# Optimization experiments

Hardware: AMD Instinct MI355X
Metric: run time of the kernel (lower is better)

## Reference

```python
import jax, jax.numpy as jnp
import numpy as np

EPS = 1e-6

def _ln(x, g, b):
    mu = jnp.mean(x, axis=-1, keepdims=True)
    var = jnp.mean(jnp.square(x - mu), axis=-1, keepdims=True)
    return (x - mu) * jax.lax.rsqrt(var + EPS) * g + b

def setup_inputs() -> dict:
    key = jax.random.key(0)
    ks = jax.random.split(key, 8)
    B, T, D = 4, 4096, 1024
    H = 16
    Dff = 4 * D
    s = 1.0 / np.sqrt(D)
    sf = 1.0 / np.sqrt(Dff)
    return {
        "x": jax.random.normal(ks[0], (B, T, D), dtype=jnp.float32),
        "wq": jax.random.uniform(ks[1], (D, D), jnp.float32, -s, s),
        "wk": jax.random.uniform(ks[2], (D, D), jnp.float32, -s, s),
        "wv": jax.random.uniform(ks[3], (D, D), jnp.float32, -s, s),
        "wo": jax.random.uniform(ks[4], (D, D), jnp.float32, -s, s),
        "ln1_g": jnp.ones((D,), jnp.float32),
        "ln1_b": jnp.zeros((D,), jnp.float32),
        "w1": jax.random.uniform(ks[5], (D, Dff), jnp.float32, -s, s),
        "b1": jnp.zeros((Dff,), jnp.float32),
        "w2": jax.random.uniform(ks[6], (Dff, D), jnp.float32, -sf, sf),
        "b2": jnp.zeros((D,), jnp.float32),
        "ln2_g": jnp.ones((D,), jnp.float32),
        "ln2_b": jnp.zeros((D,), jnp.float32),
    }

def reference(x, wq, wk, wv, wo, ln1_g, ln1_b, w1, b1, w2, b2, ln2_g, ln2_b):
    B, T, D = x.shape
    H = 16
    dk = D // H
    x1 = _ln(x, ln1_g, ln1_b)
    q = (x1 @ wq).reshape(B, T, H, dk)
    k = (x1 @ wk).reshape(B, T, H, dk)
    v = (x1 @ wv).reshape(B, T, H, dk)
    # NOTE: faithful to source -- attention mixes HEADS at each token position
    # attn[b,t,h,g] = softmax_g( sum_d q[b,t,h,d]*k[b,t,g,d] / sqrt(dk) )
    attn = jax.nn.softmax(jnp.einsum('bthd,btgd->bthg', q / np.sqrt(dk), k), axis=-1)
    o = jnp.einsum('bthg,btgd->bthd', attn, v)
    # faithful head-major reshape: transpose(1,2).contiguous().view(B,T,-1)
    o = jnp.transpose(o, (0, 2, 1, 3)).reshape(B, T, H * dk)
    o = o @ wo
    q2 = _ln(o + x, ln1_g, ln1_b)  # same layer_norm params reused
    h = jax.nn.gelu(q2 @ w1 + b1, approximate=False)
    y = h @ w2 + b2 + q2
    return _ln(y, ln2_g, ln2_b)
```

## Files before the change

kernel.cpp:

```cpp
#include <hip/hip_runtime.h>


typedef __attribute__((ext_vector_type(8))) short s16x8;
typedef __attribute__((ext_vector_type(4))) short s16x4;
typedef __attribute__((ext_vector_type(4))) float f32x4;

__device__ __forceinline__ short f2bf(float x) {
  unsigned u = __builtin_bit_cast(unsigned, x);
  u = (u + 0x7FFFu + ((u >> 16) & 1u)) >> 16;
  return (short)u;
}
__device__ __forceinline__ float bf2f(short s) {
  unsigned u = ((unsigned)(unsigned short)s) << 16;
  return __builtin_bit_cast(float, u);
}

__device__ __forceinline__ void ld_g2l16(const short* g, const short* l) {
  __builtin_amdgcn_global_load_lds(
      (const __attribute__((address_space(1))) void*)g,
      (__attribute__((address_space(3))) void*)l, 16, 0, 0);
}

__device__ __forceinline__ s16x8 lds_read8(const short* smem, int off) {
  const __attribute__((address_space(3))) short* p =
      (const __attribute__((address_space(3))) short*)smem;
  return *(const __attribute__((address_space(3))) s16x8*)(p + off);
}

__device__ __forceinline__ float fast_gelu(float v) {
  float y = 0.7978845608f * (v + 0.044715f * v * v * v);
  float ay = fabsf(y);
  float t = __expf(-2.0f * ay);
  float th = (1.0f - t) * __frcp_rn(1.0f + t);
  th = (y >= 0.f) ? th : -th;
  return 0.5f * v * (1.0f + th);
}

#define MFMA16(va, vb, vc) \
  __builtin_amdgcn_mfma_f32_16x16x32_bf16(va, vb, vc, 0, 0, 0)

template <int EPI>
__global__ __launch_bounds__(512, 2) void gemm256(
    const short* __restrict__ A, const short* __restrict__ BT,
    void* __restrict__ outp, const float* __restrict__ bias, int N, int K) {
  extern __shared__ __align__(16) short smem[];

  const int t = threadIdx.x;
  const int lane = t & 63, w = t >> 6;
  const int wm = w >> 2, wn = w & 3;

  const int nbn = N >> 8;
  const int oi = (int)blockIdx.x;
  const int seq = oi >> 3;
  const int bq = seq / nbn;
  const int bm = (oi & 7) * 8 + bq;
  const int bn = seq - bq * nbn;

  const int l8 = lane >> 3;
  const int lcw = ((lane & 7) ^ l8) * 8;
  const short* gA = A + (size_t)(bm * 256 + w * 8 + l8) * K + lcw;
  const short* gB = BT + (size_t)(bn * 256 + w * 8 + l8) * K + lcw;
  const int lb = w * 512;

  auto stage = [&](const short* g, int bufo, int h, int kt) {
    const int go = h * 128 * K + kt * 64;
    ld_g2l16(g + go, smem + bufo + h * 8192 + lb);
    ld_g2l16(g + go + 64 * K, smem + bufo + h * 8192 + 4096 + lb);
  };

  const int fr = lane & 15, fc = lane >> 4;
  const int baseA = (wm * 128 + fr) * 64;
  const int baseB = (wn * 64 + fr) * 64;
  const int sl0 = (fc ^ (fr & 7)) * 8;
  const int sl1 = ((4 + fc) ^ (fr & 7)) * 8;

  f32x4 acc[8][4];
#pragma unroll
  for (int m = 0; m < 8; ++m)
#pragma unroll
    for (int n = 0; n < 4; ++n) acc[m][n] = (f32x4){0.f, 0.f, 0.f, 0.f};

  s16x8 a[4][2], b0[2][2], b1[2][2];

  const int nt = K >> 6;

  stage(gA, 0, 0, 0);
  stage(gA, 0, 1, 0);
  stage(gB, 32768, 0, 0);
  stage(gB, 32768, 1, 0);
  if (nt > 1) {
    stage(gA, 16384, 0, 1);
    stage(gA, 16384, 1, 1);
    stage(gB, 49152, 0, 1);
    stage(gB, 49152, 1, 1);
    asm volatile("s_waitcnt vmcnt(8)" ::: "memory");
  } else {
    asm volatile("s_waitcnt vmcnt(0)" ::: "memory");
  }
  __builtin_amdgcn_s_barrier();
  asm volatile("" ::: "memory");

  for (int u = 0; u < nt; ++u) {
    const bool pf = (u + 2 < nt);
    const int pa = (u & 1) << 14;
    const int pb = 32768 + pa;

#pragma unroll
    for (int mi = 0; mi < 4; ++mi) {
      a[mi][0] = lds_read8(smem, pa + baseA + mi * 1024 + sl0);
      a[mi][1] = lds_read8(smem, pa + baseA + mi * 1024 + sl1);
    }
#pragma unroll
    for (int ni = 0; ni < 2; ++ni) {
      b0[ni][0] = lds_read8(smem, pb + baseB + ni * 1024 + sl0);
      b0[ni][1] = lds_read8(smem, pb + baseB + ni * 1024 + sl1);
    }
    __builtin_amdgcn_s_barrier();
    asm volatile("s_waitcnt lgkmcnt(0)" ::: "memory");
    __builtin_amdgcn_s_setprio(1);
#pragma unroll
    for (int mi = 0; mi < 4; ++mi)
#pragma unroll
      for (int ni = 0; ni < 2; ++ni) {
        acc[mi][ni] = MFMA16(a[mi][0], b0[ni][0], acc[mi][ni]);
        acc[mi][ni] = MFMA16(a[mi][1], b0[ni][1], acc[mi][ni]);
      }
    __builtin_amdgcn_s_setprio(0);
    __builtin_amdgcn_s_barrier();
    asm volatile("" ::: "memory");

#pragma unroll
    for (int ni = 0; ni < 2; ++ni) {
      b1[ni][0] = lds_read8(smem, pb + baseB + 2048 + ni * 1024 + sl0);
      b1[ni][1] = lds_read8(smem, pb + baseB + 2048 + ni * 1024 + sl1);
    }
    __builtin_amdgcn_s_barrier();
    asm volatile("s_waitcnt lgkmcnt(0)" ::: "memory");
    __builtin_amdgcn_s_setprio(1);
#pragma unroll
    for (int mi = 0; mi < 4; ++mi)
#pragma unroll
      for (int ni = 0; ni < 2; ++ni) {
        acc[mi][2 + ni] = MFMA16(a[mi][0], b1[ni][0], acc[mi][2 + ni]);
        acc[mi][2 + ni] = MFMA16(a[mi][1], b1[ni][1], acc[mi][2 + ni]);
      }
    __builtin_amdgcn_s_setprio(0);
    __builtin_amdgcn_s_barrier();
    asm volatile("" ::: "memory");

#pragma unroll
    for (int mi = 0; mi < 4; ++mi) {
      a[mi][0] = lds_read8(smem, pa + baseA + 4096 + mi * 1024 + sl0);
      a[mi][1] = lds_read8(smem, pa + baseA + 4096 + mi * 1024 + sl1);
    }
    if (pf) {
      stage(gB, pb, 0, u + 2);
      stage(gB, pb, 1, u + 2);
    }
    __builtin_amdgcn_s_barrier();
    asm volatile("s_waitcnt lgkmcnt(0)" ::: "memory");
    __builtin_amdgcn_s_setprio(1);
#pragma unroll
    for (int mi = 0; mi < 4; ++mi)
#pragma unroll
      for (int ni = 0; ni < 2; ++ni) {
        acc[4 + mi][2 + ni] = MFMA16(a[mi][0], b1[ni][0], acc[4 + mi][2 + ni]);
        acc[4 + mi][2 + ni] = MFMA16(a[mi][1], b1[ni][1], acc[4 + mi][2 + ni]);
      }
    __builtin_amdgcn_s_setprio(0);
    __builtin_amdgcn_s_barrier();
    asm volatile("" ::: "memory");

    if (pf) {
      stage(gA, pa, 0, u + 2);
      stage(gA, pa, 1, u + 2);
    }
    __builtin_amdgcn_s_setprio(1);
#pragma unroll
    for (int mi = 0; mi < 4; ++mi)
#pragma unroll
      for (int ni = 0; ni < 2; ++ni) {
        acc[4 + mi][ni] = MFMA16(a[mi][0], b0[ni][0], acc[4 + mi][ni]);
        acc[4 + mi][ni] = MFMA16(a[mi][1], b0[ni][1], acc[4 + mi][ni]);
      }
    __builtin_amdgcn_s_setprio(0);
    if (pf) {
      asm volatile("s_waitcnt vmcnt(8)" ::: "memory");
    } else {
      asm volatile("s_waitcnt vmcnt(0)" ::: "memory");
    }
    __builtin_amdgcn_s_barrier();
    asm volatile("" ::: "memory");
  }

  const int mb = bm * 256 + wm * 128;
  const int nb = bn * 256 + wn * 64;
  const int cr = (lane >> 4) * 4;
  const int cc = lane & 15;
#pragma unroll
  for (int m = 0; m < 8; ++m) {
#pragma unroll
    for (int n = 0; n < 4; ++n) {
#pragma unroll
      for (int r = 0; r < 4; ++r) {
        const size_t row = (size_t)(mb + m * 16 + cr + r);
        const size_t col = (size_t)(nb + n * 16 + cc);
        float v = acc[m][n][r];
        if constexpr (EPI == 0) {
          ((short*)outp)[row * N + col] = f2bf(v);
        } else if constexpr (EPI == 1) {
          ((float*)outp)[row * N + col] = v;
        } else if constexpr (EPI == 2) {
          v += bias[col];
          ((short*)outp)[row * N + col] = f2bf(fast_gelu(v));
        } else {
          float prev = ((float*)outp)[row * N + col];
          v += prev;
          if (bias) v += bias[col];
          ((float*)outp)[row * N + col] = v;
        }
      }
    }
  }
}

template <int EPI>
__global__ __launch_bounds__(512, 4) void gemm128(
    const short* __restrict__ A, const short* __restrict__ BT,
    void* __restrict__ outp, const float* __restrict__ bias, int N, int K) {
  extern __shared__ __align__(16) short smem[];

  const int t = threadIdx.x;
  const int lane = t & 63, w = t >> 6;
  const int wm = w >> 2, wn = w & 3;

  const int nbn = N >> 8;
  const int oi = (int)blockIdx.x;
  const int seq = oi >> 3;
  const int bq = seq / nbn;
  const int bm = (oi & 7) * 16 + bq;
  const int bn = seq - bq * nbn;

  const int lr = lane >> 2;
  const int lc = ((lane & 3) - ((lane >> 3) & 3)) & 3;
  const short* gA = A + (size_t)(bm * 128 + lr) * K + lc * 8;
  const short* gB = BT + (size_t)(bn * 256 + lr) * K + lc * 8;

  auto stageA = [&](int par, int kt) {
    ld_g2l16(gA + (size_t)(w * 16) * K + kt * 32, smem + par + w * 512);
  };
  auto stageB = [&](int par, int kt) {
    ld_g2l16(gB + (size_t)(2 * w * 16) * K + kt * 32,
             smem + par + 2 * w * 512);
    ld_g2l16(gB + (size_t)((2 * w + 1) * 16) * K + kt * 32,
             smem + par + (2 * w + 1) * 512);
  };

  const int fr = lane & 15, fc = lane >> 4;
  const int sl = ((fc + (fr >> 1)) & 3) * 8;
  const int baseA = (wm * 64 + fr) * 32 + sl;
  const int baseB = (wn * 64 + fr) * 32 + sl;

  f32x4 acc[4][4];
#pragma unroll
  for (int m = 0; m < 4; ++m)
#pragma unroll
    for (int n = 0; n < 4; ++n) acc[m][n] = (f32x4){0.f, 0.f, 0.f, 0.f};

  const int nt = K >> 5;

  stageA(0, 0);
  stageB(8192, 0);
  stageA(4096, 1);
  stageB(16384, 1);
  asm volatile("s_waitcnt vmcnt(3)" ::: "memory");
  __builtin_amdgcn_s_barrier();
  asm volatile("" ::: "memory");

  for (int u = 0; u < nt; ++u) {
    const bool pf = (u + 2 < nt);
    const int pA = (u & 1) * 4096;
    const int pB = 8192 + (u & 1) * 8192;

    s16x8 a[4], b[4];
#pragma unroll
    for (int i = 0; i < 4; ++i) a[i] = lds_read8(smem, pA + baseA + i * 512);
#pragma unroll
    for (int i = 0; i < 4; ++i) b[i] = lds_read8(smem, pB + baseB + i * 512);
    asm volatile("s_waitcnt lgkmcnt(0)" ::: "memory");
    __builtin_amdgcn_s_barrier();
    asm volatile("" ::: "memory");

    if (pf) {
      stageA(pA, u + 2);
      stageB(pB, u + 2);
    }
    __builtin_amdgcn_s_setprio(1);
#pragma unroll
    for (int mi = 0; mi < 4; ++mi)
#pragma unroll
      for (int ni = 0; ni < 4; ++ni)
        acc[mi][ni] = MFMA16(a[mi], b[ni], acc[mi][ni]);
    __builtin_amdgcn_s_setprio(0);
    if (pf) {
      asm volatile("s_waitcnt vmcnt(3)" ::: "memory");
    } else {
      asm volatile("s_waitcnt vmcnt(0)" ::: "memory");
    }
    __builtin_amdgcn_s_barrier();
    asm volatile("" ::: "memory");
  }

  const int mb = bm * 128 + wm * 64;
  const int nb = bn * 256 + wn * 64;
  const int cr = (lane >> 4) * 4;
  const int cc = lane & 15;
#pragma unroll
  for (int m = 0; m < 4; ++m) {
#pragma unroll
    for (int n = 0; n < 4; ++n) {
#pragma unroll
      for (int r = 0; r < 4; ++r) {
        const size_t row = (size_t)(mb + m * 16 + cr + r);
        const size_t col = (size_t)(nb + n * 16 + cc);
        float v = acc[m][n][r];
        if constexpr (EPI == 0) {
          ((short*)outp)[row * N + col] = f2bf(v);
        } else if constexpr (EPI == 1) {
          ((float*)outp)[row * N + col] = v;
        } else if constexpr (EPI == 2) {
          v += bias[col];
          ((short*)outp)[row * N + col] = f2bf(fast_gelu(v));
        } else {
          float prev = ((float*)outp)[row * N + col];
          v += prev;
          if (bias) v += bias[col];
          ((float*)outp)[row * N + col] = v;
        }
      }
    }
  }
}

__global__ __launch_bounds__(256) void ln_k(
    const float* __restrict__ in, const float* __restrict__ add,
    const float* __restrict__ g, const float* __restrict__ b,
    float* __restrict__ outf, short* __restrict__ outb) {
  const int row = blockIdx.x;
  const size_t off = (size_t)row * 1024;
  const int t = threadIdx.x;
  float4 v = ((const float4*)(in + off))[t];
  if (add) {
    float4 w = ((const float4*)(add + off))[t];
    v.x += w.x; v.y += w.y; v.z += w.z; v.w += w.w;
  }
  float s = v.x + v.y + v.z + v.w;
  float ss = v.x * v.x + v.y * v.y + v.z * v.z + v.w * v.w;
#pragma unroll
  for (int o = 32; o > 0; o >>= 1) {
    s += __shfl_xor(s, o, 64);
    ss += __shfl_xor(ss, o, 64);
  }
  __shared__ float ps[4], pss[4];
  const int lane = t & 63, wave = t >> 6;
  if (lane == 0) { ps[wave] = s; pss[wave] = ss; }
  __syncthreads();
  s = ps[0] + ps[1] + ps[2] + ps[3];
  ss = pss[0] + pss[1] + pss[2] + pss[3];
  const float mean = s * (1.0f / 1024.0f);
  const float var = ss * (1.0f / 1024.0f) - mean * mean;
  const float rstd = rsqrtf(var + 1e-6f);
  const float4 gv = ((const float4*)g)[t];
  const float4 bv = ((const float4*)b)[t];
  float4 o4;
  o4.x = (v.x - mean) * rstd * gv.x + bv.x;
  o4.y = (v.y - mean) * rstd * gv.y + bv.y;
  o4.z = (v.z - mean) * rstd * gv.z + bv.z;
  o4.w = (v.w - mean) * rstd * gv.w + bv.w;
  if (outf) ((float4*)(outf + off))[t] = o4;
  if (outb) {
    s16x4 ob;
    ob[0] = f2bf(o4.x); ob[1] = f2bf(o4.y);
    ob[2] = f2bf(o4.z); ob[3] = f2bf(o4.w);
    *(s16x4*)(outb + off + t * 4) = ob;
  }
}

__device__ __forceinline__ void wconv_tile(const float* __restrict__ W,
                                           short* __restrict__ WT, int K,
                                           int N, int n0, int k0,
                                           float (*tile)[33], int c, int r) {
#pragma unroll
  for (int rr = r; rr < 32; rr += 8)
    tile[rr][c] = W[(size_t)(k0 + rr) * N + n0 + c];
  __syncthreads();
#pragma unroll
  for (int rr = r; rr < 32; rr += 8)
    WT[(size_t)(n0 + rr) * K + k0 + c] = f2bf(tile[c][rr]);
}

__global__ __launch_bounds__(256) void wconv_all(
    const float* __restrict__ wq, const float* __restrict__ wk,
    const float* __restrict__ wv, const float* __restrict__ wo,
    const float* __restrict__ w1, const float* __restrict__ w2,
    short* __restrict__ WQKVT, short* __restrict__ WOT,
    short* __restrict__ W1T, short* __restrict__ W2aT,
    short* __restrict__ W2bT) {
  __shared__ float tile[32][33];
  const int t = threadIdx.x;
  const int c = t & 31, r = t >> 5;
  const int i = blockIdx.x;
  if (i < 4096) {
    const int seg = i >> 10, j = i & 1023;
    const int n0 = (j & 31) * 32, k0 = (j >> 5) * 32;
    const float* src = (seg == 0) ? wq : (seg == 1) ? wk : (seg == 2) ? wv : wo;
    short* dst = (seg == 3) ? WOT : WQKVT + (size_t)seg * 1024 * 1024;
    wconv_tile(src, dst, 1024, 1024, n0, k0, tile, c, r);
  } else if (i < 8192) {
    const int j = i - 4096;
    const int n0 = (j & 127) * 32, k0 = (j >> 7) * 32;
    wconv_tile(w1, W1T, 1024, 4096, n0, k0, tile, c, r);
  } else if (i < 10240) {
    const int j = i - 8192;
    const int n0 = (j & 31) * 32, k0 = (j >> 5) * 32;
    wconv_tile(w2, W2aT, 2048, 1024, n0, k0, tile, c, r);
  } else {
    const int j = i - 10240;
    const int n0 = (j & 31) * 32, k0 = (j >> 5) * 32;
    wconv_tile(w2 + (size_t)2048 * 1024, W2bT, 2048, 1024, n0, k0, tile, c, r);
  }
}

__global__ __launch_bounds__(256) void attn_k(const short* __restrict__ qkv,
                                              short* __restrict__ omix) {
  __shared__ float Qs[4][16][65];
  __shared__ float Ks[4][16][65];
  __shared__ float Vs[4][16][65];
  __shared__ float Ps[4][16][17];
  const int lane = threadIdx.x & 63;
  const int wave = threadIdx.x >> 6;
  const int tok = blockIdx.x * 4 + wave;
  const short* base = qkv + (size_t)tok * 3072;

#pragma unroll
  for (int half = 0; half < 2; half++) {
    const int e = half * 512 + lane * 8;
    const int h = e >> 6, d = e & 63;
    s16x8 rq = *(const s16x8*)(base + e);
    s16x8 rk = *(const s16x8*)(base + 1024 + e);
    s16x8 rv = *(const s16x8*)(base + 2048 + e);
#pragma unroll
    for (int j = 0; j < 8; j++) {
      Qs[wave][h][d + j] = bf2f(rq[j]);
      Ks[wave][h][d + j] = bf2f(rk[j]);
      Vs[wave][h][d + j] = bf2f(rv[j]);
    }
  }
  __syncthreads();

  const int h = lane & 15;
  const int g0 = (lane >> 4) * 4;
  float sc[4] = {0.f, 0.f, 0.f, 0.f};
  for (int d = 0; d < 64; d++) {
    const float qv = Qs[wave][h][d];
#pragma unroll
    for (int i = 0; i < 4; i++) sc[i] += qv * Ks[wave][g0 + i][d];
  }
#pragma unroll
  for (int i = 0; i < 4; i++) sc[i] *= 0.125f;
  float m = fmaxf(fmaxf(sc[0], sc[1]), fmaxf(sc[2], sc[3]));
  m = fmaxf(m, __shfl_xor(m, 16, 64));
  m = fmaxf(m, __shfl_xor(m, 32, 64));
  float e[4], sum = 0.f;
#pragma unroll
  for (int i = 0; i < 4; i++) { e[i] = __expf(sc[i] - m); sum += e[i]; }
  sum += __shfl_xor(sum, 16, 64);
  sum += __shfl_xor(sum, 32, 64);
  const float inv = __frcp_rn(sum);
#pragma unroll
  for (int i = 0; i < 4; i++) Ps[wave][h][g0 + i] = e[i] * inv;
  __syncthreads();

  const int d0 = (lane >> 4) * 16;
  float o[16];
#pragma unroll
  for (int dd = 0; dd < 16; dd++) o[dd] = 0.f;
  for (int gg = 0; gg < 16; gg++) {
    const float pv = Ps[wave][h][gg];
#pragma unroll
    for (int dd = 0; dd < 16; dd++) o[dd] += pv * Vs[wave][gg][d0 + dd];
  }

  const int b = tok >> 12, t = tok & 4095;
  const size_t dst =
      ((size_t)(b * 4096 + h * 256 + (t >> 4))) * 1024 + (t & 15) * 64 + d0;
  s16x8 w0, w1;
#pragma unroll
  for (int j = 0; j < 8; j++) { w0[j] = f2bf(o[j]); w1[j] = f2bf(o[8 + j]); }
  *(s16x8*)(omix + dst) = w0;
  *(s16x8*)(omix + dst + 8) = w1;
}

extern "C" void kernel_launch(void* const* d_in, const int* in_sizes, int n_in,
                              void* d_out, int out_size, void* d_ws,
                              size_t ws_size, hipStream_t stream) {
  const float* x    = (const float*)d_in[0];
  const float* wq   = (const float*)d_in[1];
  const float* wk   = (const float*)d_in[2];
  const float* wv   = (const float*)d_in[3];
  const float* wo   = (const float*)d_in[4];
  const float* ln1g = (const float*)d_in[5];
  const float* ln1b = (const float*)d_in[6];
  const float* w1   = (const float*)d_in[7];
  const float* b1   = (const float*)d_in[8];
  const float* w2   = (const float*)d_in[9];
  const float* b2   = (const float*)d_in[10];
  const float* ln2g = (const float*)d_in[11];
  const float* ln2b = (const float*)d_in[12];
  float* out = (float*)d_out;

  char* ws = (char*)d_ws;
  const size_t MB = 1024ull * 1024ull;
  const size_t NEEDED = 152 * MB;
  if (ws_size < NEEDED) return;

  short* QKV  = (short*)(ws + 0);
  short* Q2B  = (short*)(ws + 0);
  short* Hbuf = (short*)(ws + 32 * MB);
  short* X1 = (short*)(ws + 96 * MB);
  short* WQKVT = (short*)(ws + 128 * MB);
  short* WOT   = (short*)(ws + 134 * MB);
  short* W1T   = (short*)(ws + 136 * MB);
  short* W2aT  = (short*)(ws + 144 * MB);
  short* W2bT  = (short*)(ws + 148 * MB);

  const dim3 B256(256);
  const dim3 B512(512);
  const unsigned LDS256 = 131072;
  const unsigned LDS128 = 49152;

  static bool attr_done = false;
  if (!attr_done) {
    attr_done = true;
    void (*k0)(const short*, const short*, void*, const float*, int, int) =
        gemm256<0>;
    (void)hipFuncSetAttribute((const void*)k0,
        hipFuncAttributeMaxDynamicSharedMemorySize, (int)LDS256);
    void (*h1)(const short*, const short*, void*, const float*, int, int) =
        gemm128<1>;
    void (*h2)(const short*, const short*, void*, const float*, int, int) =
        gemm128<2>;
    void (*h4)(const short*, const short*, void*, const float*, int, int) =
        gemm128<4>;
    (void)hipFuncSetAttribute((const void*)h1,
        hipFuncAttributeMaxDynamicSharedMemorySize, (int)LDS128);
    (void)hipFuncSetAttribute((const void*)h2,
        hipFuncAttributeMaxDynamicSharedMemorySize, (int)LDS128);
    (void)hipFuncSetAttribute((const void*)h4,
        hipFuncAttributeMaxDynamicSharedMemorySize, (int)LDS128);
  }

  wconv_all<<<dim3(12288), B256, 0, stream>>>(wq, wk, wv, wo, w1, w2, WQKVT,
                                              WOT, W1T, W2aT, W2bT);

  ln_k<<<16384, B256, 0, stream>>>(x, nullptr, ln1g, ln1b, nullptr, X1);

  gemm256<0><<<dim3(768), B512, LDS256, stream>>>(X1, WQKVT, QKV, nullptr,
                                                  3072, 1024);

  attn_k<<<4096, B256, 0, stream>>>(QKV, X1);

  gemm128<1><<<dim3(512), B512, LDS128, stream>>>(X1, WOT, out, nullptr,
                                                  1024, 1024);

  ln_k<<<16384, B256, 0, stream>>>(out, x, ln1g, ln1b, out, Q2B);

  gemm128<2><<<dim3(1024), B512, LDS128, stream>>>(Q2B, W1T, Hbuf, b1,
                                                   2048, 1024);
  gemm128<4><<<dim3(512), B512, LDS128, stream>>>(Hbuf, W2aT, out, nullptr,
                                                  1024, 2048);

  gemm128<2><<<dim3(1024), B512, LDS128, stream>>>(Q2B, W1T + 2048 * 1024,
                                                   Hbuf, b1 + 2048, 2048,
                                                   1024);
  gemm128<4><<<dim3(512), B512, LDS128, stream>>>(Hbuf, W2bT, out, b2,
                                                  1024, 2048);

  ln_k<<<16384, B256, 0, stream>>>(out, nullptr, ln2g, ln2b, out, nullptr);
}
```

Measured before the change: 790.3 us.

## Hoist all LDS fragment loads per k-tile and cut GEMM barriers

The GEMM main loop now issues every LDS fragment read for a 64-wide k-tile (A halves and both B halves) up front. It then runs three MFMA blocks back to back, and only after that waits, takes one barrier, and issues both A and B global-to-LDS prefetches before the last MFMA block. This removes most of the per-quarter barriers and lgkmcnt waits that serialized LDS reads and MFMA. In exchange, more vector registers stay live (a0 and a1 together), which may lower occupancy or cause spills, and the memory issue pattern shifts.

```diff
diff --git a/kernel.cpp b/kernel.cpp
--- a/kernel.cpp
+++ b/kernel.cpp
@@ -79,8 +79,6 @@
   for (int m = 0; m < 8; ++m)
 #pragma unroll
     for (int n = 0; n < 4; ++n) acc[m][n] = (f32x4){0.f, 0.f, 0.f, 0.f};
-
-  s16x8 a[4][2], b0[2][2], b1[2][2];
 
   const int nt = K >> 6;
 
@@ -105,85 +103,73 @@
     const int pa = (u & 1) << 14;
     const int pb = 32768 + pa;
 
+    s16x8 a0[4][2], a1[4][2], b0[2][2], b1[2][2];
 #pragma unroll
     for (int mi = 0; mi < 4; ++mi) {
-      a[mi][0] = lds_read8(smem, pa + baseA + mi * 1024 + sl0);
-      a[mi][1] = lds_read8(smem, pa + baseA + mi * 1024 + sl1);
+      a0[mi][0] = lds_read8(smem, pa + baseA + mi * 1024 + sl0);
+      a0[mi][1] = lds_read8(smem, pa + baseA + mi * 1024 + sl1);
     }
 #pragma unroll
     for (int ni = 0; ni < 2; ++ni) {
       b0[ni][0] = lds_read8(smem, pb + baseB + ni * 1024 + sl0);
       b0[ni][1] = lds_read8(smem, pb + baseB + ni * 1024 + sl1);
     }
-    __builtin_amdgcn_s_barrier();
-    asm volatile("s_waitcnt lgkmcnt(0)" ::: "memory");
-    __builtin_amdgcn_s_setprio(1);
-#pragma unroll
-    for (int mi = 0; mi < 4; ++mi)
-#pragma unroll
-      for (int ni = 0; ni < 2; ++ni) {
-        acc[mi][ni] = MFMA16(a[mi][0], b0[ni][0], acc[mi][ni]);
-        acc[mi][ni] = MFMA16(a[mi][1], b0[ni][1], acc[mi][ni]);
-      }
-    __builtin_amdgcn_s_setprio(0);
-    __builtin_amdgcn_s_barrier();
-    asm volatile("" ::: "memory");
-
 #pragma unroll
     for (int ni = 0; ni < 2; ++ni) {
       b1[ni][0] = lds_read8(smem, pb + baseB + 2048 + ni * 1024 + sl0);
       b1[ni][1] = lds_read8(smem, pb + baseB + 2048 + ni * 1024 + sl1);
     }
-    __builtin_amdgcn_s_barrier();
-    asm volatile("s_waitcnt lgkmcnt(0)" ::: "memory");
+#pragma unroll
+    for (int mi = 0; mi < 4; ++mi) {
+      a1[mi][0] = lds_read8(smem, pa + baseA + 4096 + mi * 1024 + sl0);
+      a1[mi][1] = lds_read8(smem, pa + baseA + 4096 + mi * 1024 + sl1);
+    }
+
     __builtin_amdgcn_s_setprio(1);
 #pragma unroll
     for (int mi = 0; mi < 4; ++mi)
 #pragma unroll
       for (int ni = 0; ni < 2; ++ni) {
-        acc[mi][2 + ni] = MFMA16(a[mi][0], b1[ni][0], acc[mi][2 + ni]);
-        acc[mi][2 + ni] = MFMA16(a[mi][1], b1[ni][1], acc[mi][2 + ni]);
+        acc[mi][ni] = MFMA16(a0[mi][0], b0[ni][0], acc[mi][ni]);
+        acc[mi][ni] = MFMA16(a0[mi][1], b0[ni][1], acc[mi][ni]);
+      }
+#pragma unroll
+    for (int mi = 0; mi < 4; ++mi)
+#pragma unroll
+      for (int ni = 0; ni < 2; ++ni) {
+        acc[mi][2 + ni] = MFMA16(a0[mi][0], b1[ni][0], acc[mi][2 + ni]);
+        acc[mi][2 + ni] = MFMA16(a0[mi][1], b1[ni][1], acc[mi][2 + ni]);
+      }
+#pragma unroll
+    for (int mi = 0; mi < 4; ++mi)
+#pragma unroll
+      for (int ni = 0; ni < 2; ++ni) {
+        acc[4 + mi][2 + ni] = MFMA16(a1[mi][0], b1[ni][0], acc[4 + mi][2 + ni]);
+        acc[4 + mi][2 + ni] = MFMA16(a1[mi][1], b1[ni][1], acc[4 + mi][2 + ni]);
       }
     __builtin_amdgcn_s_setprio(0);
+
+    asm volatile("s_waitcnt lgkmcnt(0)" ::: "memory");
     __builtin_amdgcn_s_barrier();
     asm volatile("" ::: "memory");
 
-#pragma unroll
-    for (int mi = 0; mi < 4; ++mi) {
-      a[mi][0] = lds_read8(smem, pa + baseA + 4096 + mi * 1024 + sl0);
-      a[mi][1] = lds_read8(smem, pa + baseA + 4096 + mi * 1024 + sl1);
-    }
     if (pf) {
       stage(gB, pb, 0, u + 2);
       stage(gB, pb, 1, u + 2);
-    }
-    __builtin_amdgcn_s_barrier();
-    asm volatile("s_waitcnt lgkmcnt(0)" ::: "memory");
+      stage(gA, pa, 0, u + 2);
+      stage(gA, pa, 1, u + 2);
+    }
+
     __builtin_amdgcn_s_setprio(1);
 #pragma unroll
     for (int mi = 0; mi < 4; ++mi)
 #pragma unroll
       for (int ni = 0; ni < 2; ++ni) {
-        acc[4 + mi][2 + ni] = MFMA16(a[mi][0], b1[ni][0], acc[4 + mi][2 + ni]);
-        acc[4 + mi][2 + ni] = MFMA16(a[mi][1], b1[ni][1], acc[4 + mi][2 + ni]);
+        acc[4 + mi][ni] = MFMA16(a1[mi][0], b0[ni][0], acc[4 + mi][ni]);
+        acc[4 + mi][ni] = MFMA16(a1[mi][1], b0[ni][1], acc[4 + mi][ni]);
       }
     __builtin_amdgcn_s_setprio(0);
-    __builtin_amdgcn_s_barrier();
-    asm volatile("" ::: "memory");
-
-    if (pf) {
-      stage(gA, pa, 0, u + 2);
-      stage(gA, pa, 1, u + 2);
-    }
-    __builtin_amdgcn_s_setprio(1);
-#pragma unroll
-    for (int mi = 0; mi < 4; ++mi)
-#pragma unroll
-      for (int ni = 0; ni < 2; ++ni) {
-        acc[4 + mi][ni] = MFMA16(a[mi][0], b0[ni][0], acc[4 + mi][ni]);
-        acc[4 + mi][ni] = MFMA16(a[mi][1], b0[ni][1], acc[4 + mi][ni]);
-      }
-    __builtin_amdgcn_s_setprio(0);
+
     if (pf) {
       asm volatile("s_waitcnt vmcnt(8)" ::: "memory");
     } else {
```

Result: no change. 799.8 us (+1.2%).
